# Kernel tuning notes

Hardware: AMD Instinct MI355X
Metric: run time of the kernel (lower is better)

The kernel has to match this reference:

```python
import jax, jax.numpy as jnp
import numpy as np

OCC_THRESHOLD = 0.5  # occupancy-bitfield stand-in: cell occupied if grid value > 0.5
T_CLAMP = 1e10


def setup_inputs() -> dict:
    key = jax.random.key(0)
    k1, k2, k3 = jax.random.split(key, 3)
    R = 65536
    # origins inside the scene box [-1,1]^3 (uniform in [-0.5,0.5]^3)
    rays_o = jax.random.uniform(k1, (R, 3), dtype=jnp.float32) - 0.5
    d = jax.random.normal(k2, (R, 3), dtype=jnp.float32)
    rays_d = d / jnp.linalg.norm(d, axis=-1, keepdims=True)
    aabb = jnp.array([[-1.0, -1.0, -1.0], [1.0, 1.0, 1.0]], dtype=jnp.float32)
    density_grid = jax.random.uniform(k3, (1, 128, 128, 128), dtype=jnp.float32)
    return {"rays_o": rays_o, "rays_d": rays_d, "aabb": aabb,
            "density_grid": density_grid, "num_samples": 128}


def reference(rays_o, rays_d, aabb, density_grid, num_samples):
    R = rays_o.shape[0]
    S = int(num_samples)
    aabb_min, aabb_max = aabb[0], aabb[1]

    # ---- ray-AABB intersection (slab test), matching nerfactory_cuda.ray_aabb_intersect ----
    inv_d = 1.0 / rays_d
    t0 = (aabb_min - rays_o) * inv_d  # [R,3]
    t1 = (aabb_max - rays_o) * inv_d
    tn = jnp.max(jnp.minimum(t0, t1), axis=-1)
    tf = jnp.min(jnp.maximum(t0, t1), axis=-1)
    tn = jnp.maximum(tn, 0.0)
    miss = tf <= tn
    t_min = jnp.minimum(jnp.where(miss, T_CLAMP, tn), T_CLAMP)  # [R]
    t_max = jnp.minimum(jnp.where(miss, T_CLAMP, tf), T_CLAMP)  # [R]

    # ---- raymarching: S uniform steps in [t_min, t_max], keep occupied cells ----
    dt = jnp.where(miss, 0.0, (t_max - t_min) / S)  # [R]
    i = jnp.arange(S, dtype=rays_o.dtype)
    starts = t_min[:, None] + i * dt[:, None]        # [R,S]
    ends = starts + dt[:, None]
    t_mid = 0.5 * (starts + ends)
    pos = rays_o[:, None, :] + rays_d[:, None, :] * t_mid[..., None]  # [R,S,3]

    res = density_grid.shape[-1]
    u = (pos - aabb_min) / (aabb_max - aabb_min)  # normalized [0,1]
    cell = jnp.clip(jnp.floor(u * res).astype(jnp.int32), 0, res - 1)
    occ = density_grid[0, cell[..., 0], cell[..., 1], cell[..., 2]] > OCC_THRESHOLD
    valid = occ & (~miss[:, None]) & (dt[:, None] > 0)  # [R,S]

    # ---- stream compaction into packed buffer (fixed capacity R*S) ----
    total = R * S
    flat_valid = valid.reshape(-1)
    excl = jnp.cumsum(flat_valid.astype(jnp.int32)) - flat_valid.astype(jnp.int32)
    scatter_idx = jnp.where(flat_valid, excl, total)  # invalid -> dummy slot

    origins_b = jnp.broadcast_to(rays_o[:, None, :], (R, S, 3))
    dirs_b = jnp.broadcast_to(rays_d[:, None, :], (R, S, 3))
    vals = jnp.concatenate(
        [origins_b, dirs_b, starts[..., None], ends[..., None]], axis=-1
    ).reshape(total, 8)
    packed = jnp.zeros((total + 1, 8), dtype=vals.dtype).at[scatter_idx].set(vals)[:total]

    counts = valid.sum(axis=-1).astype(jnp.int32)        # samples per ray
    ray_start = jnp.cumsum(counts) - counts              # exclusive cumsum
    packed_info = jnp.stack([ray_start, counts], axis=-1)  # [R,2]

    # packed columns: origins(0:3), dirs(3:6), starts(6), ends(7)
    return packed, packed_info, t_min, t_max
```

## Files before the change

kernel.cpp:

```cpp
#include <hip/hip_runtime.h>

#define SAMPLES 128
#define GRID_RES 128

typedef unsigned long long u64;

__device__ __forceinline__ void slab_test(
    float ox, float oy, float oz, float dx, float dy, float dz,
    float a0, float a1, float a2, float b0, float b1, float b2,
    float& tmin, float& tmax, float& dtv, bool& miss)
{
    float ix = __fdiv_rn(1.0f, dx);
    float iy = __fdiv_rn(1.0f, dy);
    float iz = __fdiv_rn(1.0f, dz);
    float t0x = __fmul_rn(__fsub_rn(a0, ox), ix);
    float t1x = __fmul_rn(__fsub_rn(b0, ox), ix);
    float t0y = __fmul_rn(__fsub_rn(a1, oy), iy);
    float t1y = __fmul_rn(__fsub_rn(b1, oy), iy);
    float t0z = __fmul_rn(__fsub_rn(a2, oz), iz);
    float t1z = __fmul_rn(__fsub_rn(b2, oz), iz);
    float tn = fmaxf(fmaxf(fminf(t0x, t1x), fminf(t0y, t1y)), fminf(t0z, t1z));
    float tf = fminf(fminf(fmaxf(t0x, t1x), fmaxf(t0y, t1y)), fmaxf(t0z, t1z));
    tn = fmaxf(tn, 0.0f);
    miss = (tf <= tn);
    tmin = miss ? 1e10f : fminf(tn, 1e10f);
    tmax = miss ? 1e10f : fminf(tf, 1e10f);
    dtv  = miss ? 0.0f : __fdiv_rn(__fsub_rn(tmax, tmin), (float)SAMPLES);
}

__global__ __launch_bounds__(256) void k_prep(
    const float* __restrict__ grid, u64* __restrict__ bits, int ncells,
    const float* __restrict__ ro, const float* __restrict__ rd,
    const float* __restrict__ aabb,
    float* __restrict__ out_tmin, float* __restrict__ out_tmax,
    float* __restrict__ wtmin, float* __restrict__ wdt,
    unsigned* __restrict__ ctr, int R, int nbb)
{
    int b = blockIdx.x;
    int tid = threadIdx.x;
    if (b < nbb) {
        int c = b * 256 + tid;
        bool occ = (c < ncells) && (grid[c] > 0.5f);
        u64 m = __ballot(occ);
        if ((tid & 63) == 0 && c < ncells) bits[c >> 6] = m;
        return;
    }
    int r = (b - nbb) * 256 + tid;
    if (b == nbb && tid == 0) *ctr = 0u;
    if (r >= R) return;
    float ox = ro[3 * r + 0], oy = ro[3 * r + 1], oz = ro[3 * r + 2];
    float dx = rd[3 * r + 0], dy = rd[3 * r + 1], dz = rd[3 * r + 2];
    float a0 = aabb[0], a1 = aabb[1], a2 = aabb[2];
    float b0 = aabb[3], b1 = aabb[4], b2 = aabb[5];
    float tmin, tmax, dtv; bool miss;
    slab_test(ox, oy, oz, dx, dy, dz, a0, a1, a2, b0, b1, b2,
              tmin, tmax, dtv, miss);
    out_tmin[r] = tmin;
    out_tmax[r] = tmax;
    wtmin[r] = tmin;
    wdt[r]  = dtv;
}

__global__ __launch_bounds__(256) void k_pass1(
    const float* __restrict__ ro, const float* __restrict__ rd,
    const float* __restrict__ aabb, const u64* __restrict__ bits,
    const float* __restrict__ wtmin, const float* __restrict__ wdt,
    u64* __restrict__ wmask, int R)
{
    int tid = threadIdx.x;
    int ray = blockIdx.x * 2 + (tid >> 7);
    int s   = tid & 127;
    if (ray >= R) return;
    int rayu = __builtin_amdgcn_readfirstlane(ray);

    float tmin = wtmin[rayu];
    float dtv  = wdt[rayu];

    bool valid = false;
    if (dtv > 0.0f) {
        float ox = ro[3 * rayu + 0], oy = ro[3 * rayu + 1], oz = ro[3 * rayu + 2];
        float dx = rd[3 * rayu + 0], dy = rd[3 * rayu + 1], dz = rd[3 * rayu + 2];
        float a0 = aabb[0], a1 = aabb[1], a2 = aabb[2];
        float b0 = aabb[3], b1 = aabb[4], b2 = aabb[5];

        float fs    = (float)s;
        float start = __fadd_rn(tmin, __fmul_rn(fs, dtv));
        float end   = __fadd_rn(start, dtv);
        float tmid  = __fmul_rn(0.5f, __fadd_rn(start, end));
        float px = __fadd_rn(ox, __fmul_rn(dx, tmid));
        float py = __fadd_rn(oy, __fmul_rn(dy, tmid));
        float pz = __fadd_rn(oz, __fmul_rn(dz, tmid));
        float e0 = __fsub_rn(b0, a0);
        float e1 = __fsub_rn(b1, a1);
        float e2 = __fsub_rn(b2, a2);
        float ux = __fmul_rn(__fdiv_rn(__fsub_rn(px, a0), e0), (float)GRID_RES);
        float uy = __fmul_rn(__fdiv_rn(__fsub_rn(py, a1), e1), (float)GRID_RES);
        float uz = __fmul_rn(__fdiv_rn(__fsub_rn(pz, a2), e2), (float)GRID_RES);
        int cx = min(max((int)floorf(ux), 0), GRID_RES - 1);
        int cy = min(max((int)floorf(uy), 0), GRID_RES - 1);
        int cz = min(max((int)floorf(uz), 0), GRID_RES - 1);
        int idx = ((cx * GRID_RES) + cy) * GRID_RES + cz;
        valid = (bits[idx >> 6] >> (idx & 63)) & 1ull;
    }

    u64 bmask = __ballot(valid);
    if ((tid & 63) == 0) {
        wmask[(size_t)ray * 2 + (s >> 6)] = bmask;
    }
}

__global__ __launch_bounds__(1024) void k_scan(
    const u64* __restrict__ wmask, unsigned* __restrict__ lpre,
    unsigned* __restrict__ bsum, unsigned* __restrict__ boff,
    unsigned* __restrict__ wtotal, unsigned* __restrict__ ctr,
    int R, int nb)
{
    int r    = blockIdx.x * 1024 + threadIdx.x;
    int lane = threadIdx.x & 63;
    int wv   = threadIdx.x >> 6;

    unsigned c = 0;
    if (r < R)
        c = (unsigned)__popcll(wmask[2 * r]) + (unsigned)__popcll(wmask[2 * r + 1]);

    unsigned inc = c;
    for (int o = 1; o < 64; o <<= 1) {
        unsigned v = __shfl_up(inc, o, 64);
        if (lane >= o) inc += v;
    }

    __shared__ unsigned sw[16];
    __shared__ unsigned sdone;
    if (lane == 63) sw[wv] = inc;
    __syncthreads();
    if (wv == 0) {
        unsigned v = (lane < 16) ? sw[lane] : 0u;
        unsigned iv = v;
        for (int o = 1; o < 16; o <<= 1) {
            unsigned t2 = __shfl_up(iv, o, 64);
            if (lane >= o) iv += t2;
        }
        if (lane < 16) sw[lane] = iv - v;
    }
    __syncthreads();

    unsigned excl = sw[wv] + (inc - c);
    if (r < R) lpre[r] = excl;

    if (threadIdx.x == 1023) {
        atomicExch(&bsum[blockIdx.x], excl + c);
        __threadfence();
        sdone = atomicAdd(ctr, 1u);
    }
    __syncthreads();
    if (sdone == (unsigned)(nb - 1)) {
        __threadfence();
        if (threadIdx.x < 64) {
            int t = threadIdx.x;
            unsigned v = (t < nb) ? atomicAdd(&bsum[t], 0u) : 0u;
            unsigned iv = v;
            for (int o = 1; o < 64; o <<= 1) {
                unsigned u = __shfl_up(iv, o, 64);
                if (t >= o) iv += u;
            }
            if (t < nb) boff[t] = iv - v;
            if (t == 63) *wtotal = iv;
        }
    }
}

__global__ __launch_bounds__(256) void k_pack(
    const float* __restrict__ ro, const float* __restrict__ rd,
    const u64* __restrict__ wmask,
    const unsigned* __restrict__ lpre, const unsigned* __restrict__ boff,
    const float* __restrict__ wtmin, const float* __restrict__ wdt,
    const unsigned* __restrict__ wtotal,
    float* __restrict__ packed, float* __restrict__ info, int R)
{
    __shared__ unsigned sbuf[4][64 * 9];

    int tid  = threadIdx.x;
    int wv   = tid >> 6;
    int lane = tid & 63;
    int gid  = blockIdx.x * 256 + tid;
    int ray  = gid >> 7;
    int s    = gid & 127;
    int s0   = s & 64;
    int rayu = __builtin_amdgcn_readfirstlane(ray);

    u64 mlo = wmask[2 * rayu];
    u64 mhi = wmask[2 * rayu + 1];
    u64 mw  = s0 ? mhi : mlo;
    unsigned nv = (unsigned)__popcll(mw);
    unsigned wave_below = (unsigned)__popcll(mw & ((1ull << lane) - 1ull));
    bool valid = (mw >> lane) & 1ull;
    unsigned rank = valid ? wave_below : nv + ((unsigned)lane - wave_below);

    unsigned wstart = boff[rayu >> 10] + lpre[rayu];
    unsigned vbase  = wstart + (s0 ? (unsigned)__popcll(mlo) : 0u);
    unsigned wtot   = *wtotal;
    unsigned gid0   = (unsigned)(gid - lane);
    unsigned tbase  = wtot + gid0 - vbase;

    if (s == 0) {
        unsigned cnt = (unsigned)__popcll(mlo) + (unsigned)__popcll(mhi);
        info[2 * ray]     = (float)wstart;
        info[2 * ray + 1] = (float)cnt;
    }

    unsigned d0 = 0u, d1 = 0u, d2 = 0u, d3 = 0u, d4 = 0u, d5 = 0u, d6 = 0u, d7 = 0u;
    if (valid) {
        float tmin  = wtmin[rayu];
        float dtv   = wdt[rayu];
        float fs    = (float)s;
        float start = __fadd_rn(tmin, __fmul_rn(fs, dtv));
        float end   = __fadd_rn(start, dtv);
        d0 = __float_as_uint(ro[3 * rayu + 0]);
        d1 = __float_as_uint(ro[3 * rayu + 1]);
        d2 = __float_as_uint(ro[3 * rayu + 2]);
        d3 = __float_as_uint(rd[3 * rayu + 0]);
        d4 = __float_as_uint(rd[3 * rayu + 1]);
        d5 = __float_as_uint(rd[3 * rayu + 2]);
        d6 = __float_as_uint(start);
        d7 = __float_as_uint(end);
    }
    unsigned* row = &sbuf[wv][rank * 9];
    row[0] = d0; row[1] = d1; row[2] = d2; row[3] = d3;
    row[4] = d4; row[5] = d5; row[6] = d6; row[7] = d7;

    __syncthreads();

    #pragma unroll
    for (int b = 0; b < 2; ++b) {
        unsigned f = (unsigned)(b * 64 + lane);
        unsigned k = f >> 1;
        unsigned p = f & 1u;
        unsigned dest = (k < nv) ? (vbase + k) : (tbase + (k - nv));
        const unsigned* src = &sbuf[wv][k * 9 + p * 4];
        float4 val = make_float4(__uint_as_float(src[0]), __uint_as_float(src[1]),
                                 __uint_as_float(src[2]), __uint_as_float(src[3]));
        *(float4*)(packed + (size_t)dest * 8 + p * 4) = val;
    }
}

extern "C" void kernel_launch(void* const* d_in, const int* in_sizes, int n_in,
                              void* d_out, int out_size, void* d_ws, size_t ws_size,
                              hipStream_t stream)
{
    const float* ro   = (const float*)d_in[0];
    const float* rd   = (const float*)d_in[1];
    const float* aabb = (const float*)d_in[2];
    const float* grid = (const float*)d_in[3];

    int R = in_sizes[0] / 3;
    size_t total = (size_t)R * SAMPLES;
    int nb = (R + 1023) / 1024;
    int ncells = GRID_RES * GRID_RES * GRID_RES;
    int nbb = (ncells + 255) / 256;
    int nrb = (R + 255) / 256;

    float* out    = (float*)d_out;
    float* packed = out;
    float* info   = out + total * 8;
    float* otmin  = info + (size_t)2 * R;
    float* otmax  = otmin + R;

    char* w = (char*)d_ws;
    u64* wmask       = (u64*)w;
    float* wtmin     = (float*)(w + (size_t)R * 16);
    float* wdt       = wtmin + R;
    unsigned* lpre   = (unsigned*)(wdt + R);
    unsigned* bsum   = lpre + R;
    unsigned* boff   = bsum + 64;
    unsigned* wtotal = boff + 64;
    unsigned* ctr    = wtotal + 1;
    u64* bits        = (u64*)(wtotal + 63);

    k_prep<<<nbb + nrb, 256, 0, stream>>>(grid, bits, ncells, ro, rd, aabb,
                                          otmin, otmax, wtmin, wdt, ctr, R, nbb);
    int b1 = (R + 1) / 2;
    k_pass1<<<b1, 256, 0, stream>>>(ro, rd, aabb, bits, wtmin, wdt, wmask, R);
    k_scan<<<nb, 1024, 0, stream>>>(wmask, lpre, bsum, boff, wtotal, ctr, R, nb);
    int b3 = (int)(total / 256);
    k_pack<<<b3, 256, 0, stream>>>(ro, rd, wmask, lpre, boff, wtmin, wdt,
                                   wtotal, packed, info, R);
}
```

Measured before the change: 90.57 us.

## Store occupancy bitfield as 4x4x4 bricks and simplify divisions

The occupancy bitfield is rebuilt so that each 64-bit word covers a 4x4x4 brick of cells instead of 64 consecutive z-cells. Each thread builds one word from float4 loads, and the raymarch lookup indexes by brick. Neighbouring samples along a ray should then fall into the same or nearby words, which improves cache locality of the bit lookups. The change also replaces the division by 128 with a multiply by its reciprocal, and adds a fast path that multiplies by 0.5 when the box extent equals 2. Both are exact, but the prep stage now uses fewer threads, each doing more loads.

```diff
diff --git a/kernel.cpp b/kernel.cpp
--- a/kernel.cpp
+++ b/kernel.cpp
@@ -25,11 +25,11 @@
     miss = (tf <= tn);
     tmin = miss ? 1e10f : fminf(tn, 1e10f);
     tmax = miss ? 1e10f : fminf(tf, 1e10f);
-    dtv  = miss ? 0.0f : __fdiv_rn(__fsub_rn(tmax, tmin), (float)SAMPLES);
+    dtv  = miss ? 0.0f : __fmul_rn(__fsub_rn(tmax, tmin), 0.0078125f);
 }
 
 __global__ __launch_bounds__(256) void k_prep(
-    const float* __restrict__ grid, u64* __restrict__ bits, int ncells,
+    const float* __restrict__ grid, u64* __restrict__ bits,
     const float* __restrict__ ro, const float* __restrict__ rd,
     const float* __restrict__ aabb,
     float* __restrict__ out_tmin, float* __restrict__ out_tmax,
@@ -39,10 +39,24 @@
     int b = blockIdx.x;
     int tid = threadIdx.x;
     if (b < nbb) {
-        int c = b * 256 + tid;
-        bool occ = (c < ncells) && (grid[c] > 0.5f);
-        u64 m = __ballot(occ);
-        if ((tid & 63) == 0 && c < ncells) bits[c >> 6] = m;
+        int m = b * 256 + tid;
+        int BZ = m & 31, BY = (m >> 5) & 31, BX = m >> 10;
+        u64 word = 0;
+        #pragma unroll
+        for (int i = 0; i < 4; ++i) {
+            #pragma unroll
+            for (int j = 0; j < 4; ++j) {
+                const float4 v = *(const float4*)(
+                    grid + (((size_t)(BX * 4 + i) * GRID_RES + (BY * 4 + j))
+                            * GRID_RES + BZ * 4));
+                int base = (i << 4) | (j << 2);
+                if (v.x > 0.5f) word |= (1ull << (base + 0));
+                if (v.y > 0.5f) word |= (1ull << (base + 1));
+                if (v.z > 0.5f) word |= (1ull << (base + 2));
+                if (v.w > 0.5f) word |= (1ull << (base + 3));
+            }
+        }
+        bits[m] = word;
         return;
     }
     int r = (b - nbb) * 256 + tid;
@@ -61,6 +75,13 @@
     wdt[r]  = dtv;
 }
 
+__device__ __forceinline__ float norm_coord(float p, float a, float e)
+{
+    if (e == 2.0f)
+        return __fmul_rn(__fmul_rn(__fsub_rn(p, a), 0.5f), (float)GRID_RES);
+    return __fmul_rn(__fdiv_rn(__fsub_rn(p, a), e), (float)GRID_RES);
+}
+
 __global__ __launch_bounds__(256) void k_pass1(
     const float* __restrict__ ro, const float* __restrict__ rd,
     const float* __restrict__ aabb, const u64* __restrict__ bits,
@@ -90,17 +111,15 @@
         float px = __fadd_rn(ox, __fmul_rn(dx, tmid));
         float py = __fadd_rn(oy, __fmul_rn(dy, tmid));
         float pz = __fadd_rn(oz, __fmul_rn(dz, tmid));
-        float e0 = __fsub_rn(b0, a0);
-        float e1 = __fsub_rn(b1, a1);
-        float e2 = __fsub_rn(b2, a2);
-        float ux = __fmul_rn(__fdiv_rn(__fsub_rn(px, a0), e0), (float)GRID_RES);
-        float uy = __fmul_rn(__fdiv_rn(__fsub_rn(py, a1), e1), (float)GRID_RES);
-        float uz = __fmul_rn(__fdiv_rn(__fsub_rn(pz, a2), e2), (float)GRID_RES);
+        float ux = norm_coord(px, a0, __fsub_rn(b0, a0));
+        float uy = norm_coord(py, a1, __fsub_rn(b1, a1));
+        float uz = norm_coord(pz, a2, __fsub_rn(b2, a2));
         int cx = min(max((int)floorf(ux), 0), GRID_RES - 1);
         int cy = min(max((int)floorf(uy), 0), GRID_RES - 1);
         int cz = min(max((int)floorf(uz), 0), GRID_RES - 1);
-        int idx = ((cx * GRID_RES) + cy) * GRID_RES + cz;
-        valid = (bits[idx >> 6] >> (idx & 63)) & 1ull;
+        int m  = (((cx >> 2) << 5) | (cy >> 2)) * 32 + (cz >> 2);
+        int bb = ((cx & 3) << 4) | ((cy & 3) << 2) | (cz & 3);
+        valid = (bits[m] >> bb) & 1ull;
     }
 
     u64 bmask = __ballot(valid);
@@ -255,8 +274,8 @@
     int R = in_sizes[0] / 3;
     size_t total = (size_t)R * SAMPLES;
     int nb = (R + 1023) / 1024;
-    int ncells = GRID_RES * GRID_RES * GRID_RES;
-    int nbb = (ncells + 255) / 256;
+    int nbricks = 32 * 32 * 32;
+    int nbb = nbricks / 256;
     int nrb = (R + 255) / 256;
 
     float* out    = (float*)d_out;
@@ -276,7 +295,7 @@
     unsigned* ctr    = wtotal + 1;
     u64* bits        = (u64*)(wtotal + 63);
 
-    k_prep<<<nbb + nrb, 256, 0, stream>>>(grid, bits, ncells, ro, rd, aabb,
+    k_prep<<<nbb + nrb, 256, 0, stream>>>(grid, bits, ro, rd, aabb,
                                           otmin, otmax, wtmin, wdt, ctr, R, nbb);
     int b1 = (R + 1) / 2;
     k_pass1<<<b1, 256, 0, stream>>>(ro, rd, aabb, bits, wtmin, wdt, wmask, R);
```

After: 84.00 us. -7.3%, faster.
